# Kernel optimization log

Measured on AMD Instinct MI355X. Metric: run time of the kernel, lower is better.

The kernel has to match this reference:

```python
import jax, jax.numpy as jnp
import numpy as np
from jax import lax

N = 4096      # nodes
D = 256       # in_channels
H = 128       # hidden_size (cell output = 2*H = 256)
BLOCK = 128   # row-block size for the masked-max scan
THR = 0.99    # adjacency threshold on uniform A -> avg degree ~41
EPS = 1e-12


def _block_max(m, scores):
    # m: [BLOCK, N] bool, scores: [N, H] -> [BLOCK, H]
    v = jnp.where(m[:, :, None], scores[None, :, :], -jnp.inf)
    return v.max(axis=1)

_block_max = jax.checkpoint(_block_max)


def masked_max(mask, scores):
    # maxpool over neighbors, blocked over destination nodes to avoid an [N,N,H] temp
    n = mask.shape[0]
    mblk = mask.reshape(n // BLOCK, BLOCK, n)
    def body(_, m):
        return None, _block_max(m, scores)
    _, out = lax.scan(body, None, mblk)
    out = out.reshape(n, scores.shape[-1])
    # nodes with no neighbors -> 0
    return jnp.where(jnp.isneginf(out), jnp.zeros_like(out), out)


def setup_inputs() -> dict:
    key = jax.random.key(0)
    ks = jax.random.split(key, 16)
    def w(k, shape):
        fan = shape[0]
        return (jax.random.normal(k, shape, jnp.float32) / np.sqrt(fan)).astype(jnp.float32)
    D1 = 2 * H  # layer-1 input dim (= 256)
    return dict(
        x=jax.random.normal(ks[0], (N, D), jnp.float32),
        A=jax.random.uniform(ks[1], (N, N), dtype=jnp.float32),
        # layer 0 cell params
        Wp0=w(ks[2], (D, H)), bp0=jnp.zeros((H,), jnp.float32),
        Ws0=w(ks[3], (D, H)), bs0=jnp.zeros((H,), jnp.float32),
        Wn0=w(ks[4], (H, H)), bn0=jnp.zeros((H,), jnp.float32),
        # layer 1 cell params
        Wp1=w(ks[5], (D1, H)), bp1=jnp.zeros((H,), jnp.float32),
        Ws1=w(ks[6], (D1, H)), bs1=jnp.zeros((H,), jnp.float32),
        Wn1=w(ks[7], (H, H)), bn1=jnp.zeros((H,), jnp.float32),
    )


def _cell(x, mask, Wp, bp, Ws, bs, Wn, bn):
    # GraphSAGE maxpool cell: concat(self transform, neighbor maxpool transform)
    scores = jax.nn.relu(x @ Wp + bp)                 # [N, H]
    pooled = masked_max(mask, scores)                 # [N, H]
    return jnp.concatenate([x @ Ws + bs, pooled @ Wn + bn], axis=-1)  # [N, 2H]


def reference(x, A, Wp0, bp0, Ws0, bs0, Wn0, bn0, Wp1, bp1, Ws1, bs1, Wn1, bn1):
    mask = A > THR  # [N, N] bool adjacency
    for (Wp, bp, Ws, bs, Wn, bn) in ((Wp0, bp0, Ws0, bs0, Wn0, bn0),
                                     (Wp1, bp1, Ws1, bs1, Wn1, bn1)):
        x = _cell(x, mask, Wp, bp, Ws, bs, Wn, bn)
        x = jax.nn.relu(x)
        nrm = jnp.linalg.norm(x, axis=-1, keepdims=True)
        x = x / jnp.maximum(nrm, EPS)
    return x
```

## Files before the change

kernel.cpp:

```cpp
#include <hip/hip_runtime.h>

#define NN 4096
#define CAP 256
#define THRV 0.99f

typedef __attribute__((ext_vector_type(8))) short short8v;
typedef __attribute__((ext_vector_type(4))) float f32x4;

__device__ inline unsigned short f2bf(float f) {
  unsigned u = __builtin_bit_cast(unsigned, f);
  u = (u + 0x7fffu + ((u >> 16) & 1u)) >> 16;
  return (unsigned short)u;
}
__device__ inline unsigned pkmax(unsigned a, unsigned b) {
  unsigned r;
  asm("v_pk_max_u16 %0, %1, %2" : "=v"(r) : "v"(a), "v"(b));
  return r;
}
__device__ inline uint4 max4(uint4 a, uint4 b) {
  return make_uint4(pkmax(a.x, b.x), pkmax(a.y, b.y), pkmax(a.z, b.z), pkmax(a.w, b.w));
}


#define GEMM_BLKS 128
#define PREP_BLKS 96
#define SCAN_BLKS 256

__global__ __launch_bounds__(256) void kA(
    const float* __restrict__ x, const float* __restrict__ A,
    const float* __restrict__ Wp0, const float* __restrict__ bp0,
    const float* __restrict__ Ws0, const float* __restrict__ bs0,
    const float* __restrict__ Wn0, const float* __restrict__ Wp1,
    const float* __restrict__ Ws1, const float* __restrict__ Wn1,
    int* __restrict__ cnt, unsigned short* __restrict__ nbr,
    unsigned short* __restrict__ scores0, float* __restrict__ S0,
    unsigned short* __restrict__ tWn0, unsigned short* __restrict__ tWp1,
    unsigned short* __restrict__ tWs1, unsigned short* __restrict__ tWn1) {
  __shared__ union SM {
    unsigned short w[32768];
    struct { int scnt[16]; unsigned short snb[16][CAP]; } scan;
  } sm;
  const int bid = blockIdx.x;
  const int tid = threadIdx.x;

  if (bid < GEMM_BLKS) {
    const int set = bid >> 6;
    const float* W = set ? Ws0 : Wp0;
    const float* bias = set ? bs0 : bp0;
#pragma unroll
    for (int it = 0; it < 32; ++it) {
      int e0 = it * 1024 + tid * 4;
      float4 v = *(const float4*)(W + e0);
      int k = e0 >> 7, n = e0 & 127;
      int elem = (k & 3) + 4 * ((k >> 4) & 1);
      int gg = (k >> 2) & 3;
      int kt8 = (k >> 5) * 8;
      float vv[4] = {v.x, v.y, v.z, v.w};
#pragma unroll
      for (int i = 0; i < 4; ++i) {
        int nn = n + i;
        sm.w[((kt8 + (nn >> 4)) << 9) + ((gg * 16 + (nn & 15)) << 3) + elem] = f2bf(vv[i]);
      }
    }
    __syncthreads();
    const int wv = tid >> 6, lane = tid & 63;
    const int g = lane >> 4, r15 = lane & 15;
    const int rb16 = (bid & 63) * 64 + wv * 16;
    const int row = rb16 + r15;
    f32x4 acc[8] = {};
#pragma unroll
    for (int ktIdx = 0; ktIdx < 8; ++ktIdx) {
      const float* xp = x + (size_t)row * 256 + ktIdx * 32 + 4 * g;
      float4 lo = *(const float4*)xp;
      float4 hi = *(const float4*)(xp + 16);
      short8v a;
      a[0] = (short)f2bf(lo.x); a[1] = (short)f2bf(lo.y);
      a[2] = (short)f2bf(lo.z); a[3] = (short)f2bf(lo.w);
      a[4] = (short)f2bf(hi.x); a[5] = (short)f2bf(hi.y);
      a[6] = (short)f2bf(hi.z); a[7] = (short)f2bf(hi.w);
#pragma unroll
      for (int nf = 0; nf < 8; ++nf) {
        uint4 bw = *(const uint4*)(sm.w + ((ktIdx * 8 + nf) << 9) + lane * 8);
        acc[nf] = __builtin_amdgcn_mfma_f32_16x16x32_bf16(a, __builtin_bit_cast(short8v, bw), acc[nf], 0, 0, 0);
      }
    }
#pragma unroll
    for (int nf = 0; nf < 8; ++nf) {
      int col = nf * 16 + r15;
      float bv = bias[col];
#pragma unroll
      for (int r = 0; r < 4; ++r) {
        int orow = rb16 + 4 * g + r;
        float t = acc[nf][r] + bv;
        if (set == 0) scores0[(size_t)orow * 128 + col] = f2bf(fmaxf(t, 0.f));
        else          S0[(size_t)orow * 128 + col] = t;
      }
    }
    return;
  }
  if (bid < GEMM_BLKS + PREP_BLKS) {
    int id = bid - GEMM_BLKS;
    const float* src; unsigned short* dst; int base;
    if (id < 16)      { src = Wn0; dst = tWn0; base = id; }
    else if (id < 48) { src = Wp1; dst = tWp1; base = id - 16; }
    else if (id < 80) { src = Ws1; dst = tWs1; base = id - 48; }
    else              { src = Wn1; dst = tWn1; base = id - 80; }
    int e0 = base * 1024 + tid * 4;
    float4 v = *(const float4*)(src + e0);
    int k = e0 >> 7, n = e0 & 127;
    float vv[4] = {v.x, v.y, v.z, v.w};
    int elem = (k & 3) + 4 * ((k >> 4) & 1);
    int gg = (k >> 2) & 3;
    int fragkt = (k >> 5) * 8;
#pragma unroll
    for (int i = 0; i < 4; ++i) {
      int nn = n + i;
      int idx = ((fragkt + (nn >> 4)) << 9) + ((gg * 16 + (nn & 15)) << 3) + elem;
      dst[idx] = f2bf(vv[i]);
    }
    return;
  }
  {
    const int t = tid;
    const int lane = t & 63;
    const int r0 = (bid - GEMM_BLKS - PREP_BLKS) * 16;
    if (t < 16) sm.scan.scnt[t] = 0;
    __syncthreads();
    const float4* base = (const float4*)(A + (size_t)r0 * NN) + 4 * t;
    float4 c0 = base[0], c1 = base[1], c2 = base[2], c3 = base[3];
    for (int r = 0; r < 16; ++r) {
      float4 n0 = c0, n1 = c1, n2 = c2, n3 = c3;
      if (r < 15) {
        const float4* nb = base + (size_t)(r + 1) * (NN / 4);
        n0 = nb[0]; n1 = nb[1]; n2 = nb[2]; n3 = nb[3];
      }
      unsigned m = 0;
      m |= (c0.x > THRV) ? 0x1u : 0u;    m |= (c0.y > THRV) ? 0x2u : 0u;
      m |= (c0.z > THRV) ? 0x4u : 0u;    m |= (c0.w > THRV) ? 0x8u : 0u;
      m |= (c1.x > THRV) ? 0x10u : 0u;   m |= (c1.y > THRV) ? 0x20u : 0u;
      m |= (c1.z > THRV) ? 0x40u : 0u;   m |= (c1.w > THRV) ? 0x80u : 0u;
      m |= (c2.x > THRV) ? 0x100u : 0u;  m |= (c2.y > THRV) ? 0x200u : 0u;
      m |= (c2.z > THRV) ? 0x400u : 0u;  m |= (c2.w > THRV) ? 0x800u : 0u;
      m |= (c3.x > THRV) ? 0x1000u : 0u; m |= (c3.y > THRV) ? 0x2000u : 0u;
      m |= (c3.z > THRV) ? 0x4000u : 0u; m |= (c3.w > THRV) ? 0x8000u : 0u;
      int cntT = __popc(m);
      int inc = cntT;
#pragma unroll
      for (int off = 1; off < 64; off <<= 1) {
        int o = __shfl_up(inc, off, 64);
        if (lane >= off) inc += o;
      }
      int excl = inc - cntT;
      int wtot = __shfl(inc, 63, 64);
      int wbase = 0;
      if (lane == 0) wbase = atomicAdd(&sm.scan.scnt[r], wtot);
      wbase = __shfl(wbase, 0, 64);
      int pos = wbase + excl;
      while (m) {
        int i = __ffs(m) - 1;
        m &= m - 1;
        if (pos < CAP) sm.scan.snb[r][pos] = (unsigned short)(16 * t + i);
        ++pos;
      }
      c0 = n0; c1 = n1; c2 = n2; c3 = n3;
    }
    __syncthreads();
    if (t < 16) cnt[r0 + t] = min(sm.scan.scnt[t], CAP);
    {
      ushort4* dst = (ushort4*)(nbr + (size_t)r0 * CAP);
      const ushort4* s = (const ushort4*)sm.scan.snb;
#pragma unroll
      for (int i = 0; i < 4; ++i) dst[t + 256 * i] = s[t + 256 * i];
    }
  }
}

template<int LAYER>
__global__ __launch_bounds__(512) void fusedL(
    const int* __restrict__ cnt, const unsigned short* __restrict__ nbr,
    const unsigned short* __restrict__ scores_in, const float* __restrict__ S_in,
    const unsigned short* __restrict__ tWn, const float* __restrict__ bn,
    const unsigned short* __restrict__ tWp, const float* __restrict__ bp,
    const unsigned short* __restrict__ tWs, const float* __restrict__ bs,
    unsigned short* __restrict__ scores_out, float* __restrict__ S_out,
    float* __restrict__ out) {
  __shared__ int scnt[16];
  __shared__ unsigned short snb[16][CAP];
  __shared__ unsigned short pool2[16][2][136];
  __shared__ unsigned short pooled[16][136];
  __shared__ unsigned short xb[16][264];
  __shared__ float ssqs[16];
  __shared__ float ssqw[4][16];

  const int tid = threadIdx.x;
  const int wv = tid >> 6, lane = tid & 63, g = lane >> 4, r15 = lane & 15;
  const int r0 = blockIdx.x * 16;

  if (tid < 16) scnt[tid] = cnt[r0 + tid];
  {
    const ushort4* src = (const ushort4*)(nbr + (size_t)r0 * CAP);
    ushort4* dst = (ushort4*)snb;
    dst[tid] = src[tid];
    dst[tid + 512] = src[tid + 512];
  }
  __syncthreads();

  {
    const int r = tid >> 5, sub = tid & 31;
    const int h = sub >> 4, c8 = (sub & 15) * 8;
    const int c = scnt[r];
    uint4 m0 = make_uint4(0, 0, 0, 0), m1 = m0, m2 = m0, m3 = m0;
    int k = h;
    for (; k + 6 < c; k += 8) {
      int j0 = snb[r][k], j1 = snb[r][k + 2], j2 = snb[r][k + 4], j3 = snb[r][k + 6];
      uint4 a0 = *(const uint4*)(scores_in + (size_t)j0 * 128 + c8);
      uint4 a1 = *(const uint4*)(scores_in + (size_t)j1 * 128 + c8);
      uint4 a2 = *(const uint4*)(scores_in + (size_t)j2 * 128 + c8);
      uint4 a3 = *(const uint4*)(scores_in + (size_t)j3 * 128 + c8);
      m0 = max4(m0, a0); m1 = max4(m1, a1); m2 = max4(m2, a2); m3 = max4(m3, a3);
    }
    for (; k < c; k += 2)
      m0 = max4(m0, *(const uint4*)(scores_in + (size_t)snb[r][k] * 128 + c8));
    *(uint4*)&pool2[r][h][c8] = max4(max4(m0, m1), max4(m2, m3));
  }
  __syncthreads();
  if (tid < 256) {
    const int r = tid >> 4, c8 = (tid & 15) * 8;
    uint4 a = *(const uint4*)&pool2[r][0][c8];
    uint4 b = *(const uint4*)&pool2[r][1][c8];
    *(uint4*)&pooled[r][c8] = max4(a, b);
  }
  __syncthreads();

  float sv[8];
  f32x4 pacc[2] = {};
  const int srow = tid >> 4, sc8 = (tid & 15) * 8;
  if (tid < 256) {
    const float* sp = S_in + (size_t)(r0 + srow) * 128 + sc8;
    float4 sa = *(const float4*)sp;
    float4 sb = *(const float4*)(sp + 4);
    sv[0] = fmaxf(sa.x, 0.f); sv[1] = fmaxf(sa.y, 0.f);
    sv[2] = fmaxf(sa.z, 0.f); sv[3] = fmaxf(sa.w, 0.f);
    sv[4] = fmaxf(sb.x, 0.f); sv[5] = fmaxf(sb.y, 0.f);
    sv[6] = fmaxf(sb.z, 0.f); sv[7] = fmaxf(sb.w, 0.f);
    float ps = 0.f;
#pragma unroll
    for (int i = 0; i < 8; ++i) ps += sv[i] * sv[i];
#pragma unroll
    for (int off = 1; off < 16; off <<= 1) ps += __shfl_xor(ps, off, 16);
    if ((tid & 15) == 0) ssqs[srow] = ps;
  } else {
    const int wv2 = wv - 4;
#pragma unroll
    for (int kt = 0; kt < 128; kt += 32) {
      ushort4 alo = *(const ushort4*)&pooled[r15][kt + 4 * g];
      ushort4 ahi = *(const ushort4*)&pooled[r15][kt + 16 + 4 * g];
      short8v a;
      a[0] = alo.x; a[1] = alo.y; a[2] = alo.z; a[3] = alo.w;
      a[4] = ahi.x; a[5] = ahi.y; a[6] = ahi.z; a[7] = ahi.w;
#pragma unroll
      for (int f = 0; f < 2; ++f) {
        uint4 bw = *((const uint4*)(tWn + (size_t)((kt >> 5) * 8 + 2 * wv2 + f) * 512) + lane);
        pacc[f] = __builtin_amdgcn_mfma_f32_16x16x32_bf16(a, __builtin_bit_cast(short8v, bw), pacc[f], 0, 0, 0);
      }
    }
#pragma unroll
    for (int f = 0; f < 2; ++f) {
      float bv = bn[(2 * wv2 + f) * 16 + r15];
#pragma unroll
      for (int rr = 0; rr < 4; ++rr) pacc[f][rr] = fmaxf(pacc[f][rr] + bv, 0.f);
    }
#pragma unroll
    for (int rr = 0; rr < 4; ++rr) {
      float ps = pacc[0][rr] * pacc[0][rr] + pacc[1][rr] * pacc[1][rr];
#pragma unroll
      for (int off = 1; off < 16; off <<= 1) ps += __shfl_xor(ps, off, 16);
      if (r15 == 0) ssqw[wv2][4 * g + rr] = ps;
    }
  }
  __syncthreads();

  if (LAYER == 0) {
    if (tid < 256) {
      float tot = ssqs[srow] + ssqw[0][srow] + ssqw[1][srow] + ssqw[2][srow] + ssqw[3][srow];
      float sc = 1.f / fmaxf(sqrtf(tot), 1e-12f);
      unsigned short hh[8];
#pragma unroll
      for (int i = 0; i < 8; ++i) hh[i] = f2bf(sv[i] * sc);
      uint4 wvv;
      wvv.x = (unsigned)hh[0] | ((unsigned)hh[1] << 16);
      wvv.y = (unsigned)hh[2] | ((unsigned)hh[3] << 16);
      wvv.z = (unsigned)hh[4] | ((unsigned)hh[5] << 16);
      wvv.w = (unsigned)hh[6] | ((unsigned)hh[7] << 16);
      *(uint4*)&xb[srow][sc8] = wvv;
    } else {
      const int wv2 = wv - 4;
#pragma unroll
      for (int rr = 0; rr < 4; ++rr) {
        int row = 4 * g + rr;
        float tot = ssqs[row] + ssqw[0][row] + ssqw[1][row] + ssqw[2][row] + ssqw[3][row];
        float sc = 1.f / fmaxf(sqrtf(tot), 1e-12f);
#pragma unroll
        for (int f = 0; f < 2; ++f)
          xb[row][128 + (2 * wv2 + f) * 16 + r15] = f2bf(pacc[f][rr] * sc);
      }
    }
    __syncthreads();
    const int s = wv >> 2;
    const unsigned short* Wt = s ? tWs : tWp;
    const float* bb = s ? bs : bp;
    const int nf0 = (wv & 3) * 2;
    f32x4 dacc[2] = {};
#pragma unroll
    for (int kt = 0; kt < 256; kt += 32) {
      ushort4 alo = *(const ushort4*)&xb[r15][kt + 4 * g];
      ushort4 ahi = *(const ushort4*)&xb[r15][kt + 16 + 4 * g];
      short8v a;
      a[0] = alo.x; a[1] = alo.y; a[2] = alo.z; a[3] = alo.w;
      a[4] = ahi.x; a[5] = ahi.y; a[6] = ahi.z; a[7] = ahi.w;
#pragma unroll
      for (int f = 0; f < 2; ++f) {
        uint4 bw = *((const uint4*)(Wt + (size_t)((kt >> 5) * 8 + nf0 + f) * 512) + lane);
        dacc[f] = __builtin_amdgcn_mfma_f32_16x16x32_bf16(a, __builtin_bit_cast(short8v, bw), dacc[f], 0, 0, 0);
      }
    }
#pragma unroll
    for (int f = 0; f < 2; ++f) {
      int col = (nf0 + f) * 16 + r15;
      float bv = bb[col];
#pragma unroll
      for (int rr = 0; rr < 4; ++rr) {
        int grow = r0 + 4 * g + rr;
        float t = dacc[f][rr] + bv;
        if (s == 0) scores_out[(size_t)grow * 128 + col] = f2bf(fmaxf(t, 0.f));
        else        S_out[(size_t)grow * 128 + col] = t;
      }
    }
  } else {
    if (tid < 256) {
      float tot = ssqs[srow] + ssqw[0][srow] + ssqw[1][srow] + ssqw[2][srow] + ssqw[3][srow];
      float sc = 1.f / fmaxf(sqrtf(tot), 1e-12f);
      float* op = out + (size_t)(r0 + srow) * 256 + sc8;
      *(float4*)op = make_float4(sv[0] * sc, sv[1] * sc, sv[2] * sc, sv[3] * sc);
      *(float4*)(op + 4) = make_float4(sv[4] * sc, sv[5] * sc, sv[6] * sc, sv[7] * sc);
    } else {
      const int wv2 = wv - 4;
#pragma unroll
      for (int rr = 0; rr < 4; ++rr) {
        int row = 4 * g + rr;
        float tot = ssqs[row] + ssqw[0][row] + ssqw[1][row] + ssqw[2][row] + ssqw[3][row];
        float sc = 1.f / fmaxf(sqrtf(tot), 1e-12f);
#pragma unroll
        for (int f = 0; f < 2; ++f)
          out[(size_t)(r0 + row) * 256 + 128 + (2 * wv2 + f) * 16 + r15] = pacc[f][rr] * sc;
      }
    }
  }
}

extern "C" void kernel_launch(void* const* d_in, const int* in_sizes, int n_in,
                              void* d_out, int out_size, void* d_ws, size_t ws_size,
                              hipStream_t stream) {
  (void)in_sizes; (void)n_in; (void)out_size; (void)ws_size;
  const float* x   = (const float*)d_in[0];
  const float* A   = (const float*)d_in[1];
  const float* Wp0 = (const float*)d_in[2];
  const float* bp0 = (const float*)d_in[3];
  const float* Ws0 = (const float*)d_in[4];
  const float* bs0 = (const float*)d_in[5];
  const float* Wn0 = (const float*)d_in[6];
  const float* bn0 = (const float*)d_in[7];
  const float* Wp1 = (const float*)d_in[8];
  const float* bp1 = (const float*)d_in[9];
  const float* Ws1 = (const float*)d_in[10];
  const float* bs1 = (const float*)d_in[11];
  const float* Wn1 = (const float*)d_in[12];
  const float* bn1 = (const float*)d_in[13];

  char* ws = (char*)d_ws;
  auto alloc = [&](size_t bytes) { char* p = ws; ws += (bytes + 255) & ~(size_t)255; return p; };
  int* cnt             = (int*)alloc((size_t)NN * 4);
  unsigned short* nbr  = (unsigned short*)alloc((size_t)NN * CAP * 2);
  unsigned short* tWn0 = (unsigned short*)alloc(128 * 128 * 2);
  unsigned short* tWp1 = (unsigned short*)alloc(256 * 128 * 2);
  unsigned short* tWs1 = (unsigned short*)alloc(256 * 128 * 2);
  unsigned short* tWn1 = (unsigned short*)alloc(128 * 128 * 2);
  unsigned short* scores0 = (unsigned short*)alloc((size_t)NN * 128 * 2);
  unsigned short* scores1 = (unsigned short*)alloc((size_t)NN * 128 * 2);
  float* S0            = (float*)alloc((size_t)NN * 128 * 4);
  float* S1            = (float*)alloc((size_t)NN * 128 * 4);

  kA<<<GEMM_BLKS + PREP_BLKS + SCAN_BLKS, 256, 0, stream>>>(
      x, A, Wp0, bp0, Ws0, bs0, Wn0, Wp1, Ws1, Wn1,
      cnt, nbr, scores0, S0, tWn0, tWp1, tWs1, tWn1);
  fusedL<0><<<NN / 16, 512, 0, stream>>>(cnt, nbr, scores0, S0,
                                         tWn0, bn0, tWp1, bp1, tWs1, bs1,
                                         scores1, S1, nullptr);
  fusedL<1><<<NN / 16, 512, 0, stream>>>(cnt, nbr, scores1, S1,
                                         tWn1, bn1, nullptr, nullptr, nullptr, nullptr,
                                         nullptr, nullptr, (float*)d_out);
}
```

Baseline: 44.38 us.

## Shrink kA shared memory, split scan into more blocks, reorder block roles

```diff
diff --git a/kernel.cpp b/kernel.cpp
--- a/kernel.cpp
+++ b/kernel.cpp
@@ -22,9 +22,9 @@
 }
 
 
+#define SCAN_BLKS 512
+#define PREP_BLKS 96
 #define GEMM_BLKS 128
-#define PREP_BLKS 96
-#define SCAN_BLKS 256
 
 __global__ __launch_bounds__(256) void kA(
     const float* __restrict__ x, const float* __restrict__ A,
@@ -37,69 +37,67 @@
     unsigned short* __restrict__ tWn0, unsigned short* __restrict__ tWp1,
     unsigned short* __restrict__ tWs1, unsigned short* __restrict__ tWn1) {
   __shared__ union SM {
-    unsigned short w[32768];
-    struct { int scnt[16]; unsigned short snb[16][CAP]; } scan;
+    unsigned short w[16384];
+    struct { int scnt[8]; unsigned short snb[8][CAP]; } scan;
   } sm;
   const int bid = blockIdx.x;
   const int tid = threadIdx.x;
 
-  if (bid < GEMM_BLKS) {
-    const int set = bid >> 6;
-    const float* W = set ? Ws0 : Wp0;
-    const float* bias = set ? bs0 : bp0;
-#pragma unroll
-    for (int it = 0; it < 32; ++it) {
-      int e0 = it * 1024 + tid * 4;
-      float4 v = *(const float4*)(W + e0);
-      int k = e0 >> 7, n = e0 & 127;
-      int elem = (k & 3) + 4 * ((k >> 4) & 1);
-      int gg = (k >> 2) & 3;
-      int kt8 = (k >> 5) * 8;
-      float vv[4] = {v.x, v.y, v.z, v.w};
-#pragma unroll
-      for (int i = 0; i < 4; ++i) {
-        int nn = n + i;
-        sm.w[((kt8 + (nn >> 4)) << 9) + ((gg * 16 + (nn & 15)) << 3) + elem] = f2bf(vv[i]);
-      }
-    }
+  if (bid < SCAN_BLKS) {
+    const int lane = tid & 63;
+    const int r0 = bid * 8;
+    if (tid < 8) sm.scan.scnt[tid] = 0;
     __syncthreads();
-    const int wv = tid >> 6, lane = tid & 63;
-    const int g = lane >> 4, r15 = lane & 15;
-    const int rb16 = (bid & 63) * 64 + wv * 16;
-    const int row = rb16 + r15;
-    f32x4 acc[8] = {};
-#pragma unroll
-    for (int ktIdx = 0; ktIdx < 8; ++ktIdx) {
-      const float* xp = x + (size_t)row * 256 + ktIdx * 32 + 4 * g;
-      float4 lo = *(const float4*)xp;
-      float4 hi = *(const float4*)(xp + 16);
-      short8v a;
-      a[0] = (short)f2bf(lo.x); a[1] = (short)f2bf(lo.y);
-      a[2] = (short)f2bf(lo.z); a[3] = (short)f2bf(lo.w);
-      a[4] = (short)f2bf(hi.x); a[5] = (short)f2bf(hi.y);
-      a[6] = (short)f2bf(hi.z); a[7] = (short)f2bf(hi.w);
-#pragma unroll
-      for (int nf = 0; nf < 8; ++nf) {
-        uint4 bw = *(const uint4*)(sm.w + ((ktIdx * 8 + nf) << 9) + lane * 8);
-        acc[nf] = __builtin_amdgcn_mfma_f32_16x16x32_bf16(a, __builtin_bit_cast(short8v, bw), acc[nf], 0, 0, 0);
-      }
-    }
-#pragma unroll
-    for (int nf = 0; nf < 8; ++nf) {
-      int col = nf * 16 + r15;
-      float bv = bias[col];
-#pragma unroll
-      for (int r = 0; r < 4; ++r) {
-        int orow = rb16 + 4 * g + r;
-        float t = acc[nf][r] + bv;
-        if (set == 0) scores0[(size_t)orow * 128 + col] = f2bf(fmaxf(t, 0.f));
-        else          S0[(size_t)orow * 128 + col] = t;
-      }
+    const float4* base = (const float4*)(A + (size_t)r0 * NN) + 4 * tid;
+    float4 c0 = base[0], c1 = base[1], c2 = base[2], c3 = base[3];
+    for (int r = 0; r < 8; ++r) {
+      float4 n0 = c0, n1 = c1, n2 = c2, n3 = c3;
+      if (r < 7) {
+        const float4* nb = base + (size_t)(r + 1) * (NN / 4);
+        n0 = nb[0]; n1 = nb[1]; n2 = nb[2]; n3 = nb[3];
+      }
+      unsigned m = 0;
+      m |= (c0.x > THRV) ? 0x1u : 0u;    m |= (c0.y > THRV) ? 0x2u : 0u;
+      m |= (c0.z > THRV) ? 0x4u : 0u;    m |= (c0.w > THRV) ? 0x8u : 0u;
+      m |= (c1.x > THRV) ? 0x10u : 0u;   m |= (c1.y > THRV) ? 0x20u : 0u;
+      m |= (c1.z > THRV) ? 0x40u : 0u;   m |= (c1.w > THRV) ? 0x80u : 0u;
+      m |= (c2.x > THRV) ? 0x100u : 0u;  m |= (c2.y > THRV) ? 0x200u : 0u;
+      m |= (c2.z > THRV) ? 0x400u : 0u;  m |= (c2.w > THRV) ? 0x800u : 0u;
+      m |= (c3.x > THRV) ? 0x1000u : 0u; m |= (c3.y > THRV) ? 0x2000u : 0u;
+      m |= (c3.z > THRV) ? 0x4000u : 0u; m |= (c3.w > THRV) ? 0x8000u : 0u;
+      int cntT = __popc(m);
+      int inc = cntT;
+#pragma unroll
+      for (int off = 1; off < 64; off <<= 1) {
+        int o = __shfl_up(inc, off, 64);
+        if (lane >= off) inc += o;
+      }
+      int excl = inc - cntT;
+      int wtot = __shfl(inc, 63, 64);
+      int wbase = 0;
+      if (lane == 0) wbase = atomicAdd(&sm.scan.scnt[r], wtot);
+      wbase = __shfl(wbase, 0, 64);
+      int pos = wbase + excl;
+      while (m) {
+        int i = __ffs(m) - 1;
+        m &= m - 1;
+        if (pos < CAP) sm.scan.snb[r][pos] = (unsigned short)(16 * tid + i);
+        ++pos;
+      }
+      c0 = n0; c1 = n1; c2 = n2; c3 = n3;
+    }
+    __syncthreads();
+    if (tid < 8) cnt[r0 + tid] = min(sm.scan.scnt[tid], CAP);
+    {
+      ushort4* dst = (ushort4*)(nbr + (size_t)r0 * CAP);
+      const ushort4* s = (const ushort4*)sm.scan.snb;
+      dst[tid] = s[tid];
+      dst[tid + 256] = s[tid + 256];
     }
     return;
   }
-  if (bid < GEMM_BLKS + PREP_BLKS) {
-    int id = bid - GEMM_BLKS;
+  if (bid < SCAN_BLKS + PREP_BLKS) {
+    int id = bid - SCAN_BLKS;
     const float* src; unsigned short* dst; int base;
     if (id < 16)      { src = Wn0; dst = tWn0; base = id; }
     else if (id < 48) { src = Wp1; dst = tWp1; base = id - 16; }
@@ -121,56 +119,62 @@
     return;
   }
   {
-    const int t = tid;
-    const int lane = t & 63;
-    const int r0 = (bid - GEMM_BLKS - PREP_BLKS) * 16;
-    if (t < 16) sm.scan.scnt[t] = 0;
-    __syncthreads();
-    const float4* base = (const float4*)(A + (size_t)r0 * NN) + 4 * t;
-    float4 c0 = base[0], c1 = base[1], c2 = base[2], c3 = base[3];
-    for (int r = 0; r < 16; ++r) {
-      float4 n0 = c0, n1 = c1, n2 = c2, n3 = c3;
-      if (r < 15) {
-        const float4* nb = base + (size_t)(r + 1) * (NN / 4);
-        n0 = nb[0]; n1 = nb[1]; n2 = nb[2]; n3 = nb[3];
-      }
-      unsigned m = 0;
-      m |= (c0.x > THRV) ? 0x1u : 0u;    m |= (c0.y > THRV) ? 0x2u : 0u;
-      m |= (c0.z > THRV) ? 0x4u : 0u;    m |= (c0.w > THRV) ? 0x8u : 0u;
-      m |= (c1.x > THRV) ? 0x10u : 0u;   m |= (c1.y > THRV) ? 0x20u : 0u;
-      m |= (c1.z > THRV) ? 0x40u : 0u;   m |= (c1.w > THRV) ? 0x80u : 0u;
-      m |= (c2.x > THRV) ? 0x100u : 0u;  m |= (c2.y > THRV) ? 0x200u : 0u;
-      m |= (c2.z > THRV) ? 0x400u : 0u;  m |= (c2.w > THRV) ? 0x800u : 0u;
-      m |= (c3.x > THRV) ? 0x1000u : 0u; m |= (c3.y > THRV) ? 0x2000u : 0u;
-      m |= (c3.z > THRV) ? 0x4000u : 0u; m |= (c3.w > THRV) ? 0x8000u : 0u;
-      int cntT = __popc(m);
-      int inc = cntT;
-#pragma unroll
-      for (int off = 1; off < 64; off <<= 1) {
-        int o = __shfl_up(inc, off, 64);
-        if (lane >= off) inc += o;
-      }
-      int excl = inc - cntT;
-      int wtot = __shfl(inc, 63, 64);
-      int wbase = 0;
-      if (lane == 0) wbase = atomicAdd(&sm.scan.scnt[r], wtot);
-      wbase = __shfl(wbase, 0, 64);
-      int pos = wbase + excl;
-      while (m) {
-        int i = __ffs(m) - 1;
-        m &= m - 1;
-        if (pos < CAP) sm.scan.snb[r][pos] = (unsigned short)(16 * t + i);
-        ++pos;
-      }
-      c0 = n0; c1 = n1; c2 = n2; c3 = n3;
-    }
-    __syncthreads();
-    if (t < 16) cnt[r0 + t] = min(sm.scan.scnt[t], CAP);
-    {
-      ushort4* dst = (ushort4*)(nbr + (size_t)r0 * CAP);
-      const ushort4* s = (const ushort4*)sm.scan.snb;
-#pragma unroll
-      for (int i = 0; i < 4; ++i) dst[t + 256 * i] = s[t + 256 * i];
+    const int gb = bid - SCAN_BLKS - PREP_BLKS;
+    const int set = gb >> 6;
+    const float* W = set ? Ws0 : Wp0;
+    const float* bias = set ? bs0 : bp0;
+    const int wv = tid >> 6, lane = tid & 63;
+    const int g = lane >> 4, r15 = lane & 15;
+    const int rb16 = (gb & 63) * 64 + wv * 16;
+    const int row = rb16 + r15;
+    f32x4 acc[8] = {};
+#pragma unroll
+    for (int pass = 0; pass < 2; ++pass) {
+#pragma unroll
+      for (int it = 0; it < 16; ++it) {
+        int e0 = it * 1024 + tid * 4;
+        float4 v = *(const float4*)(W + pass * 16384 + e0);
+        int kl = e0 >> 7, n = e0 & 127;
+        int elem = (kl & 3) + 4 * ((kl >> 4) & 1);
+        int gg = (kl >> 2) & 3;
+        int kt8 = (kl >> 5) * 8;
+        float vv[4] = {v.x, v.y, v.z, v.w};
+#pragma unroll
+        for (int i = 0; i < 4; ++i) {
+          int nn = n + i;
+          sm.w[((kt8 + (nn >> 4)) << 9) + ((gg * 16 + (nn & 15)) << 3) + elem] = f2bf(vv[i]);
+        }
+      }
+      __syncthreads();
+#pragma unroll
+      for (int ktl = 0; ktl < 4; ++ktl) {
+        const float* xp = x + (size_t)row * 256 + pass * 128 + ktl * 32 + 4 * g;
+        float4 lo = *(const float4*)xp;
+        float4 hi = *(const float4*)(xp + 16);
+        short8v a;
+        a[0] = (short)f2bf(lo.x); a[1] = (short)f2bf(lo.y);
+        a[2] = (short)f2bf(lo.z); a[3] = (short)f2bf(lo.w);
+        a[4] = (short)f2bf(hi.x); a[5] = (short)f2bf(hi.y);
+        a[6] = (short)f2bf(hi.z); a[7] = (short)f2bf(hi.w);
+#pragma unroll
+        for (int nf = 0; nf < 8; ++nf) {
+          uint4 bw = *(const uint4*)(sm.w + ((ktl * 8 + nf) << 9) + lane * 8);
+          acc[nf] = __builtin_amdgcn_mfma_f32_16x16x32_bf16(a, __builtin_bit_cast(short8v, bw), acc[nf], 0, 0, 0);
+        }
+      }
+      __syncthreads();
+    }
+#pragma unroll
+    for (int nf = 0; nf < 8; ++nf) {
+      int col = nf * 16 + r15;
+      float bv = bias[col];
+#pragma unroll
+      for (int r = 0; r < 4; ++r) {
+        int orow = rb16 + 4 * g + r;
+        float t = acc[nf][r] + bv;
+        if (set == 0) scores0[(size_t)orow * 128 + col] = f2bf(fmaxf(t, 0.f));
+        else          S0[(size_t)orow * 128 + col] = t;
+      }
     }
   }
 }
@@ -390,7 +394,7 @@
   float* S0            = (float*)alloc((size_t)NN * 128 * 4);
   float* S1            = (float*)alloc((size_t)NN * 128 * 4);
 
-  kA<<<GEMM_BLKS + PREP_BLKS + SCAN_BLKS, 256, 0, stream>>>(
+  kA<<<SCAN_BLKS + PREP_BLKS + GEMM_BLKS, 256, 0, stream>>>(
       x, A, Wp0, bp0, Ws0, bs0, Wn0, Wp1, Ws1, Wn1,
       cnt, nbr, scores0, S0, tWn0, tWp1, tWs1, tWn1);
   fusedL<0><<<NN / 16, 512, 0, stream>>>(cnt, nbr, scores0, S0,
```

New measurement: 50.12 us. 12.9% more time.

## Split adjacency scan into its own finer-grained kernel separate from GEMM/prep

Applied to the files above, without the earlier changes.

```diff
diff --git a/kernel.cpp b/kernel.cpp
--- a/kernel.cpp
+++ b/kernel.cpp
@@ -22,28 +22,73 @@
 }
 
 
-#define GEMM_BLKS 128
-#define PREP_BLKS 96
-#define SCAN_BLKS 256
-
-__global__ __launch_bounds__(256) void kA(
-    const float* __restrict__ x, const float* __restrict__ A,
+__global__ __launch_bounds__(256) void k_scan(
+    const float* __restrict__ A, int* __restrict__ cnt, unsigned short* __restrict__ nbr) {
+  __shared__ int scnt[4];
+  __shared__ unsigned short snb[4][CAP];
+  const int tid = threadIdx.x;
+  const int lane = tid & 63;
+  const int r0 = blockIdx.x * 4;
+  if (tid < 4) scnt[tid] = 0;
+  __syncthreads();
+  const float4* base = (const float4*)(A + (size_t)r0 * NN) + 4 * tid;
+  float4 c0 = base[0], c1 = base[1], c2 = base[2], c3 = base[3];
+#pragma unroll
+  for (int r = 0; r < 4; ++r) {
+    float4 n0 = c0, n1 = c1, n2 = c2, n3 = c3;
+    if (r < 3) {
+      const float4* nb = base + (size_t)(r + 1) * (NN / 4);
+      n0 = nb[0]; n1 = nb[1]; n2 = nb[2]; n3 = nb[3];
+    }
+    unsigned m = 0;
+    m |= (c0.x > THRV) ? 0x1u : 0u;    m |= (c0.y > THRV) ? 0x2u : 0u;
+    m |= (c0.z > THRV) ? 0x4u : 0u;    m |= (c0.w > THRV) ? 0x8u : 0u;
+    m |= (c1.x > THRV) ? 0x10u : 0u;   m |= (c1.y > THRV) ? 0x20u : 0u;
+    m |= (c1.z > THRV) ? 0x40u : 0u;   m |= (c1.w > THRV) ? 0x80u : 0u;
+    m |= (c2.x > THRV) ? 0x100u : 0u;  m |= (c2.y > THRV) ? 0x200u : 0u;
+    m |= (c2.z > THRV) ? 0x400u : 0u;  m |= (c2.w > THRV) ? 0x800u : 0u;
+    m |= (c3.x > THRV) ? 0x1000u : 0u; m |= (c3.y > THRV) ? 0x2000u : 0u;
+    m |= (c3.z > THRV) ? 0x4000u : 0u; m |= (c3.w > THRV) ? 0x8000u : 0u;
+    int cntT = __popc(m);
+    int inc = cntT;
+#pragma unroll
+    for (int off = 1; off < 64; off <<= 1) {
+      int o = __shfl_up(inc, off, 64);
+      if (lane >= off) inc += o;
+    }
+    int excl = inc - cntT;
+    int wtot = __shfl(inc, 63, 64);
+    int wbase = 0;
+    if (lane == 0) wbase = atomicAdd(&scnt[r], wtot);
+    wbase = __shfl(wbase, 0, 64);
+    int pos = wbase + excl;
+    while (m) {
+      int i = __ffs(m) - 1;
+      m &= m - 1;
+      if (pos < CAP) snb[r][pos] = (unsigned short)(16 * tid + i);
+      ++pos;
+    }
+    c0 = n0; c1 = n1; c2 = n2; c3 = n3;
+  }
+  __syncthreads();
+  if (tid < 4) cnt[r0 + tid] = min(scnt[tid], CAP);
+  ((ushort4*)(nbr + (size_t)r0 * CAP))[tid] = ((const ushort4*)snb)[tid];
+}
+
+__global__ __launch_bounds__(256) void k_gp(
+    const float* __restrict__ x,
     const float* __restrict__ Wp0, const float* __restrict__ bp0,
     const float* __restrict__ Ws0, const float* __restrict__ bs0,
     const float* __restrict__ Wn0, const float* __restrict__ Wp1,
     const float* __restrict__ Ws1, const float* __restrict__ Wn1,
-    int* __restrict__ cnt, unsigned short* __restrict__ nbr,
     unsigned short* __restrict__ scores0, float* __restrict__ S0,
     unsigned short* __restrict__ tWn0, unsigned short* __restrict__ tWp1,
     unsigned short* __restrict__ tWs1, unsigned short* __restrict__ tWn1) {
-  __shared__ union SM {
-    unsigned short w[32768];
-    struct { int scnt[16]; unsigned short snb[16][CAP]; } scan;
-  } sm;
+  __shared__ unsigned short smw[32768];
   const int bid = blockIdx.x;
   const int tid = threadIdx.x;
 
-  if (bid < GEMM_BLKS) {
+  if (bid < 128) {
     const int set = bid >> 6;
     const float* W = set ? Ws0 : Wp0;
     const float* bias = set ? bs0 : bp0;
@@ -59,7 +104,7 @@
 #pragma unroll
       for (int i = 0; i < 4; ++i) {
         int nn = n + i;
-        sm.w[((kt8 + (nn >> 4)) << 9) + ((gg * 16 + (nn & 15)) << 3) + elem] = f2bf(vv[i]);
+        smw[((kt8 + (nn >> 4)) << 9) + ((gg * 16 + (nn & 15)) << 3) + elem] = f2bf(vv[i]);
       }
     }
     __syncthreads();
@@ -80,7 +125,7 @@
       a[6] = (short)f2bf(hi.z); a[7] = (short)f2bf(hi.w);
 #pragma unroll
       for (int nf = 0; nf < 8; ++nf) {
-        uint4 bw = *(const uint4*)(sm.w + ((ktIdx * 8 + nf) << 9) + lane * 8);
+        uint4 bw = *(const uint4*)(smw + ((ktIdx * 8 + nf) << 9) + lane * 8);
         acc[nf] = __builtin_amdgcn_mfma_f32_16x16x32_bf16(a, __builtin_bit_cast(short8v, bw), acc[nf], 0, 0, 0);
       }
     }
@@ -98,80 +143,24 @@
     }
     return;
   }
-  if (bid < GEMM_BLKS + PREP_BLKS) {
-    int id = bid - GEMM_BLKS;
-    const float* src; unsigned short* dst; int base;
-    if (id < 16)      { src = Wn0; dst = tWn0; base = id; }
-    else if (id < 48) { src = Wp1; dst = tWp1; base = id - 16; }
-    else if (id < 80) { src = Ws1; dst = tWs1; base = id - 48; }
-    else              { src = Wn1; dst = tWn1; base = id - 80; }
-    int e0 = base * 1024 + tid * 4;
-    float4 v = *(const float4*)(src + e0);
-    int k = e0 >> 7, n = e0 & 127;
-    float vv[4] = {v.x, v.y, v.z, v.w};
-    int elem = (k & 3) + 4 * ((k >> 4) & 1);
-    int gg = (k >> 2) & 3;
-    int fragkt = (k >> 5) * 8;
-#pragma unroll
-    for (int i = 0; i < 4; ++i) {
-      int nn = n + i;
-      int idx = ((fragkt + (nn >> 4)) << 9) + ((gg * 16 + (nn & 15)) << 3) + elem;
-      dst[idx] = f2bf(vv[i]);
-    }
-    return;
-  }
-  {
-    const int t = tid;
-    const int lane = t & 63;
-    const int r0 = (bid - GEMM_BLKS - PREP_BLKS) * 16;
-    if (t < 16) sm.scan.scnt[t] = 0;
-    __syncthreads();
-    const float4* base = (const float4*)(A + (size_t)r0 * NN) + 4 * t;
-    float4 c0 = base[0], c1 = base[1], c2 = base[2], c3 = base[3];
-    for (int r = 0; r < 16; ++r) {
-      float4 n0 = c0, n1 = c1, n2 = c2, n3 = c3;
-      if (r < 15) {
-        const float4* nb = base + (size_t)(r + 1) * (NN / 4);
-        n0 = nb[0]; n1 = nb[1]; n2 = nb[2]; n3 = nb[3];
-      }
-      unsigned m = 0;
-      m |= (c0.x > THRV) ? 0x1u : 0u;    m |= (c0.y > THRV) ? 0x2u : 0u;
-      m |= (c0.z > THRV) ? 0x4u : 0u;    m |= (c0.w > THRV) ? 0x8u : 0u;
-      m |= (c1.x > THRV) ? 0x10u : 0u;   m |= (c1.y > THRV) ? 0x20u : 0u;
-      m |= (c1.z > THRV) ? 0x40u : 0u;   m |= (c1.w > THRV) ? 0x80u : 0u;
-      m |= (c2.x > THRV) ? 0x100u : 0u;  m |= (c2.y > THRV) ? 0x200u : 0u;
-      m |= (c2.z > THRV) ? 0x400u : 0u;  m |= (c2.w > THRV) ? 0x800u : 0u;
-      m |= (c3.x > THRV) ? 0x1000u : 0u; m |= (c3.y > THRV) ? 0x2000u : 0u;
-      m |= (c3.z > THRV) ? 0x4000u : 0u; m |= (c3.w > THRV) ? 0x8000u : 0u;
-      int cntT = __popc(m);
-      int inc = cntT;
-#pragma unroll
-      for (int off = 1; off < 64; off <<= 1) {
-        int o = __shfl_up(inc, off, 64);
-        if (lane >= off) inc += o;
-      }
-      int excl = inc - cntT;
-      int wtot = __shfl(inc, 63, 64);
-      int wbase = 0;
-      if (lane == 0) wbase = atomicAdd(&sm.scan.scnt[r], wtot);
-      wbase = __shfl(wbase, 0, 64);
-      int pos = wbase + excl;
-      while (m) {
-        int i = __ffs(m) - 1;
-        m &= m - 1;
-        if (pos < CAP) sm.scan.snb[r][pos] = (unsigned short)(16 * t + i);
-        ++pos;
-      }
-      c0 = n0; c1 = n1; c2 = n2; c3 = n3;
-    }
-    __syncthreads();
-    if (t < 16) cnt[r0 + t] = min(sm.scan.scnt[t], CAP);
-    {
-      ushort4* dst = (ushort4*)(nbr + (size_t)r0 * CAP);
-      const ushort4* s = (const ushort4*)sm.scan.snb;
-#pragma unroll
-      for (int i = 0; i < 4; ++i) dst[t + 256 * i] = s[t + 256 * i];
-    }
+  int id = bid - 128;
+  const float* src; unsigned short* dst; int base;
+  if (id < 16)      { src = Wn0; dst = tWn0; base = id; }
+  else if (id < 48) { src = Wp1; dst = tWp1; base = id - 16; }
+  else if (id < 80) { src = Ws1; dst = tWs1; base = id - 48; }
+  else              { src = Wn1; dst = tWn1; base = id - 80; }
+  int e0 = base * 1024 + tid * 4;
+  float4 v = *(const float4*)(src + e0);
+  int k = e0 >> 7, n = e0 & 127;
+  float vv[4] = {v.x, v.y, v.z, v.w};
+  int elem = (k & 3) + 4 * ((k >> 4) & 1);
+  int gg = (k >> 2) & 3;
+  int fragkt = (k >> 5) * 8;
+#pragma unroll
+  for (int i = 0; i < 4; ++i) {
+    int nn = n + i;
+    int idx = ((fragkt + (nn >> 4)) << 9) + ((gg * 16 + (nn & 15)) << 3) + elem;
+    dst[idx] = f2bf(vv[i]);
   }
 }
 
@@ -390,9 +379,9 @@
   float* S0            = (float*)alloc((size_t)NN * 128 * 4);
   float* S1            = (float*)alloc((size_t)NN * 128 * 4);
 
-  kA<<<GEMM_BLKS + PREP_BLKS + SCAN_BLKS, 256, 0, stream>>>(
-      x, A, Wp0, bp0, Ws0, bs0, Wn0, Wp1, Ws1, Wn1,
-      cnt, nbr, scores0, S0, tWn0, tWp1, tWs1, tWn1);
+  k_scan<<<NN / 4, 256, 0, stream>>>(A, cnt, nbr);
+  k_gp<<<224, 256, 0, stream>>>(x, Wp0, bp0, Ws0, bs0, Wn0, Wp1, Ws1, Wn1,
+                                scores0, S0, tWn0, tWp1, tWs1, tWn1);
   fusedL<0><<<NN / 16, 512, 0, stream>>>(cnt, nbr, scores0, S0,
                                          tWn0, bn0, tWp1, bp1, tWs1, bs1,
                                          scores1, S1, nullptr);
```

Result: slower. 51.08 us (+15.1%).

## Split adjacency scan between prep kernel and layer-0 fused kernel

Applied to the files above, without the earlier changes.

```diff
diff --git a/kernel.cpp b/kernel.cpp
--- a/kernel.cpp
+++ b/kernel.cpp
@@ -3,6 +3,7 @@
 #define NN 4096
 #define CAP 256
 #define THRV 0.99f
+#define PRE 100
 
 typedef __attribute__((ext_vector_type(8))) short short8v;
 typedef __attribute__((ext_vector_type(4))) float f32x4;
@@ -24,7 +25,7 @@
 
 #define GEMM_BLKS 128
 #define PREP_BLKS 96
-#define SCAN_BLKS 256
+#define SCAN_BLKS PRE
 
 __global__ __launch_bounds__(256) void kA(
     const float* __restrict__ x, const float* __restrict__ A,
@@ -177,7 +178,8 @@
 
 template<int LAYER>
 __global__ __launch_bounds__(512) void fusedL(
-    const int* __restrict__ cnt, const unsigned short* __restrict__ nbr,
+    const float* __restrict__ A,
+    int* __restrict__ cnt, unsigned short* __restrict__ nbr,
     const unsigned short* __restrict__ scores_in, const float* __restrict__ S_in,
     const unsigned short* __restrict__ tWn, const float* __restrict__ bn,
     const unsigned short* __restrict__ tWp, const float* __restrict__ bp,
@@ -196,14 +198,62 @@
   const int wv = tid >> 6, lane = tid & 63, g = lane >> 4, r15 = lane & 15;
   const int r0 = blockIdx.x * 16;
 
-  if (tid < 16) scnt[tid] = cnt[r0 + tid];
-  {
-    const ushort4* src = (const ushort4*)(nbr + (size_t)r0 * CAP);
-    ushort4* dst = (ushort4*)snb;
-    dst[tid] = src[tid];
-    dst[tid + 512] = src[tid + 512];
-  }
-  __syncthreads();
+  if (LAYER == 0 && blockIdx.x >= PRE) {
+    if (tid < 16) scnt[tid] = 0;
+    __syncthreads();
+    const float4* Ar = (const float4*)(A + (size_t)r0 * NN);
+    float4 c0 = Ar[tid], c1 = Ar[tid + 512];
+    for (int r = 0; r < 16; ++r) {
+      float4 n0 = c0, n1 = c1;
+      if (r < 15) {
+        const float4* nx = Ar + (size_t)(r + 1) * (NN / 4);
+        n0 = nx[tid]; n1 = nx[tid + 512];
+      }
+      unsigned m = 0;
+      m |= (c0.x > THRV) ? 0x1u : 0u;  m |= (c0.y > THRV) ? 0x2u : 0u;
+      m |= (c0.z > THRV) ? 0x4u : 0u;  m |= (c0.w > THRV) ? 0x8u : 0u;
+      m |= (c1.x > THRV) ? 0x10u : 0u; m |= (c1.y > THRV) ? 0x20u : 0u;
+      m |= (c1.z > THRV) ? 0x40u : 0u; m |= (c1.w > THRV) ? 0x80u : 0u;
+      int cntT = __popc(m);
+      int inc = cntT;
+#pragma unroll
+      for (int off = 1; off < 64; off <<= 1) {
+        int o = __shfl_up(inc, off, 64);
+        if (lane >= off) inc += o;
+      }
+      int excl = inc - cntT;
+      int wtot = __shfl(inc, 63, 64);
+      int wbase = 0;
+      if (lane == 0) wbase = atomicAdd(&scnt[r], wtot);
+      wbase = __shfl(wbase, 0, 64);
+      int pos = wbase + excl;
+      while (m) {
+        int b = __ffs(m) - 1;
+        m &= m - 1;
+        if (pos < CAP) snb[r][pos] = (unsigned short)(4 * tid + 2048 * (b >> 2) + (b & 3));
+        ++pos;
+      }
+      c0 = n0; c1 = n1;
+    }
+    __syncthreads();
+    if (tid < 16) { int c = min(scnt[tid], CAP); scnt[tid] = c; cnt[r0 + tid] = c; }
+    __syncthreads();
+    {
+      ushort4* dst = (ushort4*)(nbr + (size_t)r0 * CAP);
+      const ushort4* s = (const ushort4*)snb;
+      dst[tid] = s[tid];
+      dst[tid + 512] = s[tid + 512];
+    }
+  } else {
+    if (tid < 16) scnt[tid] = cnt[r0 + tid];
+    {
+      const ushort4* src = (const ushort4*)(nbr + (size_t)r0 * CAP);
+      ushort4* dst = (ushort4*)snb;
+      dst[tid] = src[tid];
+      dst[tid + 512] = src[tid + 512];
+    }
+    __syncthreads();
+  }
 
   {
     const int r = tid >> 5, sub = tid & 31;
@@ -393,10 +443,10 @@
   kA<<<GEMM_BLKS + PREP_BLKS + SCAN_BLKS, 256, 0, stream>>>(
       x, A, Wp0, bp0, Ws0, bs0, Wn0, Wp1, Ws1, Wn1,
       cnt, nbr, scores0, S0, tWn0, tWp1, tWs1, tWn1);
-  fusedL<0><<<NN / 16, 512, 0, stream>>>(cnt, nbr, scores0, S0,
+  fusedL<0><<<NN / 16, 512, 0, stream>>>(A, cnt, nbr, scores0, S0,
                                          tWn0, bn0, tWp1, bp1, tWs1, bs1,
                                          scores1, S1, nullptr);
-  fusedL<1><<<NN / 16, 512, 0, stream>>>(cnt, nbr, scores1, S1,
+  fusedL<1><<<NN / 16, 512, 0, stream>>>(A, cnt, nbr, scores1, S1,
                                          tWn1, bn1, nullptr, nullptr, nullptr, nullptr,
                                          nullptr, nullptr, (float*)d_out);
 }
```

New measurement: 54.66 us. +23.2%, slower.
